# Optimization experiments

Hardware: AMD Instinct MI355X
Metric: run time of the kernel (lower is better)

Reference implementation:

```python
import jax, jax.numpy as jnp
import numpy as np

N_NODES = 100000
N_EDGES = 3200000
IN_DIM, HID, OUT = 512, 256, 64


def setup_inputs() -> dict:
    key = jax.random.key(0)
    k1, k2, k3, k4, k5, k6 = jax.random.split(key, 6)
    x = jax.random.normal(k1, (N_NODES, IN_DIM), dtype=jnp.float32)
    edge_src = jax.random.randint(k2, (N_EDGES,), 0, N_NODES, dtype=jnp.int32)
    edge_dst = jax.random.randint(k3, (N_EDGES,), 0, N_NODES, dtype=jnp.int32)
    edge_val = jax.random.uniform(k4, (N_EDGES,), dtype=jnp.float32)
    # glorot init as in the original `glorot([input_dim, output_dim])`
    w1 = jax.random.normal(k5, (IN_DIM, HID), dtype=jnp.float32) * np.sqrt(2.0 / (IN_DIM + HID))
    w2 = jax.random.normal(k6, (HID, OUT), dtype=jnp.float32) * np.sqrt(2.0 / (HID + OUT))
    return {"x": x, "edge_src": edge_src, "edge_dst": edge_dst,
            "edge_val": edge_val, "w1": w1, "w2": w2}


def _spmm(edge_src, edge_dst, edge_val, dense):
    # support @ dense : out[i] = sum_j A[i,j] * dense[j], A given as COO edges
    msgs = edge_val[:, None] * dense[edge_dst]            # [E, D] gather
    return jax.ops.segment_sum(msgs, edge_src, num_segments=N_NODES)  # scatter-add


def reference(x, edge_src, edge_dst, edge_val, w1, w2):
    # Layer 1: pre_sup = X @ W1 ; support = A @ pre_sup ; relu (no bias)
    h = jax.nn.relu(_spmm(edge_src, edge_dst, edge_val, x @ w1))  # [N, HID]
    # Layer 2: identity activation
    logits = _spmm(edge_src, edge_dst, edge_val, h @ w2)          # [N, OUT]
    return logits
```

## Files before the change

### kernel.cpp

```cpp
#include <hip/hip_runtime.h>

#define NN 100000
#define NE 3200000
#define IN_DIM 512
#define HID 256
#define OUTD 64
#define NB 196
#define CAP 20480
#define EPB 3125

typedef _Float16 f16x8 __attribute__((ext_vector_type(8)));
typedef float f32x4 __attribute__((ext_vector_type(4)));

__device__ __forceinline__ void async_copy16(void* lds, const void* g) {
    __builtin_amdgcn_global_load_lds(
        (const __attribute__((address_space(1))) void*)g,
        (__attribute__((address_space(3))) void*)lds, 16, 0, 0);
}

__device__ __forceinline__ void dq4(int w, float m, float* a) {
    int lo = (w & 0x00ff00ff) | 0x64006400;
    int hi = ((w >> 8) & 0x00ff00ff) | 0x64006400;
    asm("v_fma_mix_f32 %0, %1, %2, %0 op_sel:[0,0,0] op_sel_hi:[1,0,0]" : "+v"(a[0]) : "v"(lo), "v"(m));
    asm("v_fma_mix_f32 %0, %1, %2, %0 op_sel:[0,0,0] op_sel_hi:[1,0,0]" : "+v"(a[1]) : "v"(hi), "v"(m));
    asm("v_fma_mix_f32 %0, %1, %2, %0 op_sel:[1,0,0] op_sel_hi:[1,0,0]" : "+v"(a[2]) : "v"(lo), "v"(m));
    asm("v_fma_mix_f32 %0, %1, %2, %0 op_sel:[1,0,0] op_sel_hi:[1,0,0]" : "+v"(a[3]) : "v"(hi), "v"(m));
}


__global__ void prep_kernel(const float* __restrict__ w1, const float* __restrict__ w2,
                            _Float16* __restrict__ w1t, _Float16* __restrict__ w2t,
                            int* __restrict__ cursor) {
    int idx = blockIdx.x * blockDim.x + threadIdx.x;
    if (idx < NB) cursor[idx] = idx * CAP;
    if (idx < IN_DIM * HID) {
        int k = idx / HID, n = idx % HID;
        w1t[(size_t)n * IN_DIM + k] = (_Float16)w1[idx];
    } else if (idx < IN_DIM * HID + HID * OUTD) {
        int j = idx - IN_DIM * HID;
        int k = j / OUTD, n = j % OUTD;
        w2t[(size_t)n * HID + k] = (_Float16)w2[j];
    }
}


__global__ __launch_bounds__(256) void bin_kernel(const int* __restrict__ src,
                                                  const int* __restrict__ dst,
                                                  const float* __restrict__ val,
                                                  int* __restrict__ cursor,
                                                  int2* __restrict__ pairs_tmp,
                                                  int E) {
    __shared__ int s_src[EPB];
    __shared__ int s_dst[EPB];
    __shared__ int s_val[EPB];
    __shared__ int hist[NB];
    __shared__ int base[NB];
    const int t = threadIdx.x;
    const int lo = blockIdx.x * EPB;
    const int cnt = min(E - lo, EPB);
    for (int i = t; i < NB; i += 256) hist[i] = 0;
    for (int i = t; i < cnt; i += 256) {
        s_src[i] = src[lo + i];
        s_dst[i] = dst[lo + i];
        s_val[i] = __float_as_int(val[lo + i]);
    }
    __syncthreads();
    for (int i = t; i < cnt; i += 256) atomicAdd(&hist[s_src[i] >> 9], 1);
    __syncthreads();
    for (int i = t; i < NB; i += 256) {
        base[i] = atomicAdd(&cursor[i], hist[i]);
        hist[i] = 0;
    }
    __syncthreads();
    for (int i = t; i < cnt; i += 256) {
        int s = s_src[i];
        int b = s >> 9;
        int l = atomicAdd(&hist[b], 1);
        int pos = base[b] + l;
        pairs_tmp[pos] = make_int2(s_dst[i] | ((s & 511) << 20), s_val[i]);
    }
}


__global__ void bucket_scan_kernel(const int* __restrict__ cursor,
                                   int* __restrict__ bbase, int* __restrict__ offs) {
    __shared__ int sz[NB];
    int t = threadIdx.x;
    if (t < NB) sz[t] = cursor[t] - t * CAP;
    __syncthreads();
    if (t == 0) {
        int acc = 0;
        for (int i = 0; i < NB; ++i) { bbase[i] = acc; acc += sz[i]; }
        bbase[NB] = acc;
        offs[NN] = acc;
    }
}


#define CSR_LDS 18432
__global__ __launch_bounds__(1024) void csr_kernel(const int* __restrict__ cursor,
                                                   const int* __restrict__ bbase,
                                                   const int2* __restrict__ pairs_tmp,
                                                   const float* __restrict__ scales,
                                                   int* __restrict__ offs,
                                                   int2* __restrict__ pairs) {
    __shared__ int sx[CSR_LDS];
    __shared__ int sv[CSR_LDS];
    __shared__ int cnt[512];
    __shared__ int wsum[8];
    const int b = blockIdx.x;
    const int t = threadIdx.x;
    const int s0 = b << 9;
    const int base = bbase[b];
    const int n_b = cursor[b] - b * CAP;
    const int tlo = b * CAP;
    if (t < 512) cnt[t] = 0;
    __syncthreads();
    for (int i = t; i < n_b; i += 1024) {
        int2 pv = pairs_tmp[tlo + i];
        sx[i] = pv.x;
        sv[i] = pv.y;
        atomicAdd(&cnt[((unsigned)pv.x) >> 20], 1);
    }
    __syncthreads();
    int my = 0, incl = 0;
    if (t < 512) {
        my = cnt[t];
        incl = my;
        #pragma unroll
        for (int d = 1; d < 64; d <<= 1) {
            int y = __shfl_up(incl, d);
            if ((t & 63) >= d) incl += y;
        }
        if ((t & 63) == 63) wsum[t >> 6] = incl;
    }
    __syncthreads();
    if (t == 0) {
        int acc = 0;
        #pragma unroll
        for (int i = 0; i < 8; ++i) { int v = wsum[i]; wsum[i] = acc; acc += v; }
    }
    __syncthreads();
    if (t < 512) {
        int excl = base + incl - my + wsum[t >> 6];
        int s = s0 + t;
        if (s < NN) offs[s] = excl;
        cnt[t] = excl;
    }
    __syncthreads();
    for (int i = t; i < n_b; i += 1024) {
        int x = sx[i];
        int so = ((unsigned)x) >> 20;
        int p = atomicAdd(&cnt[so], 1);
        int dst = x & 0xFFFFF;
        float v = __int_as_float(sv[i]) * scales[dst];
        pairs[p] = make_int2(dst, __float_as_int(v));
    }
}


__global__ __launch_bounds__(256) void gemm1_f32a(const float* __restrict__ A,
                                                  const _Float16* __restrict__ Bt,
                                                  unsigned char* __restrict__ qC,
                                                  float* __restrict__ scales,
                                                  int M) {
    __shared__ float    As[128 * 32];
    __shared__ _Float16 Bs[256 * 32];
    __shared__ float    rmaxl[2][128];
    const int tid  = threadIdx.x;
    const int lane = tid & 63;
    const int wave = tid >> 6;
    const int wm = wave >> 1, wn = wave & 1;
    const int m0 = blockIdx.x * 128;

    f32x4 acc[4][8];
    #pragma unroll
    for (int i = 0; i < 4; ++i)
        #pragma unroll
        for (int j = 0; j < 8; ++j) acc[i][j] = (f32x4){0.f, 0.f, 0.f, 0.f};

    for (int k0 = 0; k0 < IN_DIM; k0 += 32) {
        #pragma unroll
        for (int it = 0; it < 4; ++it) {
            int i = it * 256 + tid;
            int r = i >> 3;
            int cp = i & 7;
            int cl = cp ^ (r & 7);
            int gr = m0 + r; if (gr >= M) gr = M - 1;
            async_copy16((char*)As + i * 16, A + (size_t)gr * IN_DIM + k0 + cl * 4);
        }
        #pragma unroll
        for (int it = 0; it < 4; ++it) {
            int i = it * 256 + tid;
            int r = i >> 2;
            int cp = i & 3;
            int cl = cp ^ (r & 3);
            async_copy16((char*)Bs + i * 16, Bt + (size_t)r * IN_DIM + k0 + cl * 8);
        }
        __syncthreads();

        const int kc = lane >> 4;
        f16x8 af[4];
        #pragma unroll
        for (int m = 0; m < 4; ++m) {
            int r = wm * 64 + m * 16 + (lane & 15);
            int p0 = (2 * kc) ^ (r & 7);
            int p1 = (2 * kc + 1) ^ (r & 7);
            f32x4 c0 = *(const f32x4*)((const char*)As + r * 128 + p0 * 16);
            f32x4 c1 = *(const f32x4*)((const char*)As + r * 128 + p1 * 16);
            f16x8 v = { (_Float16)c0[0], (_Float16)c0[1], (_Float16)c0[2], (_Float16)c0[3],
                        (_Float16)c1[0], (_Float16)c1[1], (_Float16)c1[2], (_Float16)c1[3] };
            af[m] = v;
        }
        f16x8 bf[8];
        #pragma unroll
        for (int n = 0; n < 8; ++n) {
            int r = wn * 128 + n * 16 + (lane & 15);
            bf[n] = *(const f16x8*)((const char*)Bs + r * 64 + ((kc ^ (r & 3)) * 16));
        }
        #pragma unroll
        for (int m = 0; m < 4; ++m)
            #pragma unroll
            for (int n = 0; n < 8; ++n)
                acc[m][n] = __builtin_amdgcn_mfma_f32_16x16x32_f16(af[m], bf[n], acc[m][n], 0, 0, 0);
        __syncthreads();
    }

    #pragma unroll
    for (int m = 0; m < 4; ++m)
        #pragma unroll
        for (int r = 0; r < 4; ++r) {
            float mm = 0.f;
            #pragma unroll
            for (int n = 0; n < 8; ++n) mm = fmaxf(mm, fabsf(acc[m][n][r]));
            #pragma unroll
            for (int d = 1; d < 16; d <<= 1) mm = fmaxf(mm, __shfl_xor(mm, d));
            if ((lane & 15) == 0)
                rmaxl[wn][wm * 64 + m * 16 + (lane >> 4) * 4 + r] = mm;
        }
    __syncthreads();
    #pragma unroll
    for (int m = 0; m < 4; ++m)
        #pragma unroll
        for (int r = 0; r < 4; ++r) {
            int lrow = wm * 64 + m * 16 + (lane >> 4) * 4 + r;
            int row = m0 + lrow;
            float full = fmaxf(fmaxf(rmaxl[0][lrow], rmaxl[1][lrow]), 1e-12f);
            float inv = 127.0f / full;
            if (row < M) {
                #pragma unroll
                for (int n = 0; n < 8; ++n) {
                    int col = wn * 128 + n * 16 + (lane & 15);
                    qC[(size_t)row * HID + col] =
                        (unsigned char)(__float2int_rn(acc[m][n][r] * inv) + 128);
                }
                if (wn == 0 && (lane & 15) == 0) scales[row] = full * (1.0f / 127.0f);
            }
        }
}


__global__ __launch_bounds__(256) void spmm_relu_mm2(const int* __restrict__ offs,
                                                     const int2* __restrict__ pairs,
                                                     const unsigned char* __restrict__ qpre,
                                                     const float* __restrict__ scales,
                                                     const _Float16* __restrict__ w2t,
                                                     unsigned char* __restrict__ qh2,
                                                     float* __restrict__ ratio2, int n) {
    __shared__ __align__(16) char hl_raw[16 * 528];
    __shared__ float rmax2[4][16];
    const int tid  = threadIdx.x;
    const int lane = tid & 63;
    const int wid  = tid >> 6;
    const int par  = lane >> 4;
    const int fl   = lane & 15;
    const int nbase = blockIdx.x * 16;
    const unsigned char* qbase = qpre + fl * 16;

    #pragma unroll 1
    for (int i = 0; i < 4; ++i) {
        const int node = nbase + wid * 4 + i;
        const int beg = offs[node], end = offs[node + 1];
        float a[16] = {};
        float msum = 0.f;
        int k = beg;
        for (; k + 16 <= end; k += 16) {
            int2 pr[4];
            #pragma unroll
            for (int j = 0; j < 4; ++j) pr[j] = pairs[k + 4 * j + par];
            int4 qv[4];
            #pragma unroll
            for (int j = 0; j < 4; ++j)
                qv[j] = *(const int4*)(qbase + (size_t)pr[j].x * HID);
            #pragma unroll
            for (int j = 0; j < 4; ++j) {
                float m = __int_as_float(pr[j].y);
                msum += m;
                dq4(qv[j].x, m, a + 0);
                dq4(qv[j].y, m, a + 4);
                dq4(qv[j].z, m, a + 8);
                dq4(qv[j].w, m, a + 12);
            }
        }
        if (k < end) {
            int2 pr[4];
            float m_[4];
            #pragma unroll
            for (int j = 0; j < 4; ++j) {
                int idx = k + 4 * j + par;
                int cidx = idx < end ? idx : end - 1;
                pr[j] = pairs[cidx];
                m_[j] = idx < end ? __int_as_float(pr[j].y) : 0.f;
            }
            int4 qv[4];
            #pragma unroll
            for (int j = 0; j < 4; ++j)
                qv[j] = *(const int4*)(qbase + (size_t)pr[j].x * HID);
            #pragma unroll
            for (int j = 0; j < 4; ++j) {
                float m = m_[j];
                msum += m;
                dq4(qv[j].x, m, a + 0);
                dq4(qv[j].y, m, a + 4);
                dq4(qv[j].z, m, a + 8);
                dq4(qv[j].w, m, a + 12);
            }
        }
        #pragma unroll
        for (int q = 0; q < 16; ++q) {
            a[q] += __shfl_xor(a[q], 16);
            a[q] += __shfl_xor(a[q], 32);
        }
        msum += __shfl_xor(msum, 16);
        msum += __shfl_xor(msum, 32);
        if (par == 0) {
            float bias = 1152.f * msum;
            f16x8 o0, o1;
            #pragma unroll
            for (int q = 0; q < 8; ++q) {
                o0[q] = (_Float16)fmaxf(a[q] - bias, 0.f);
                o1[q] = (_Float16)fmaxf(a[8 + q] - bias, 0.f);
            }
            char* bp = hl_raw + (wid * 4 + i) * 528 + fl * 16;
            *(f16x8*)bp         = o0;
            *(f16x8*)(bp + 256) = o1;
        }
    }
    __syncthreads();

    const int r  = lane & 15;
    const int kc = lane >> 4;
    f32x4 acc = (f32x4){0.f, 0.f, 0.f, 0.f};
    #pragma unroll
    for (int kk = 0; kk < 8; ++kk) {
        int c = kk * 4 + kc;
        f16x8 af = *(const f16x8*)(hl_raw + r * 528 + ((c & 1) << 8) + ((c >> 1) << 4));
        f16x8 bf = *(const f16x8*)(w2t + (size_t)(wid * 16 + r) * HID + kk * 32 + kc * 8);
        acc = __builtin_amdgcn_mfma_f32_16x16x32_f16(af, bf, acc, 0, 0, 0);
    }
    float mxv[4];
    #pragma unroll
    for (int j = 0; j < 4; ++j) {
        float mm = fabsf(acc[j]);
        #pragma unroll
        for (int d = 1; d < 16; d <<= 1) mm = fmaxf(mm, __shfl_xor(mm, d));
        mxv[j] = mm;
    }
    if (r == 0) {
        #pragma unroll
        for (int j = 0; j < 4; ++j) rmax2[wid][kc * 4 + j] = mxv[j];
    }
    __syncthreads();
    #pragma unroll
    for (int j = 0; j < 4; ++j) {
        int ln = kc * 4 + j;
        int node = nbase + ln;
        float full = fmaxf(fmaxf(fmaxf(rmax2[0][ln], rmax2[1][ln]),
                                 fmaxf(rmax2[2][ln], rmax2[3][ln])), 1e-12f);
        qh2[(size_t)node * OUTD + wid * 16 + r] =
            (unsigned char)(__float2int_rn(acc[j] * (127.0f / full)) + 128);
        if (wid == 0 && r == 0)
            ratio2[node] = full * (1.0f / 127.0f) / scales[node];
    }
}


__global__ __launch_bounds__(256) void spmm64_q(const int* __restrict__ offs,
                                                const int2* __restrict__ pairs,
                                                const unsigned char* __restrict__ qh2,
                                                const float* __restrict__ ratio2,
                                                float* __restrict__ out, int n) {
    int node = blockIdx.x * 4 + (threadIdx.x >> 6);
    if (node >= n) return;
    int lane = threadIdx.x & 63;
    int par = lane >> 2;
    int fl  = lane & 3;
    int beg = offs[node], end = offs[node + 1];
    const unsigned char* qbase = qh2 + fl * 16;
    float a[16] = {};
    float msum = 0.f;
    int k = beg;
    for (; k + 32 <= end; k += 32) {
        int2 pr[2];
        #pragma unroll
        for (int j = 0; j < 2; ++j) pr[j] = pairs[k + 16 * j + par];
        float rt[2];
        #pragma unroll
        for (int j = 0; j < 2; ++j) rt[j] = ratio2[pr[j].x];
        int4 qv[2];
        #pragma unroll
        for (int j = 0; j < 2; ++j)
            qv[j] = *(const int4*)(qbase + (size_t)pr[j].x * OUTD);
        #pragma unroll
        for (int j = 0; j < 2; ++j) {
            float m = __int_as_float(pr[j].y) * rt[j];
            msum += m;
            dq4(qv[j].x, m, a + 0);
            dq4(qv[j].y, m, a + 4);
            dq4(qv[j].z, m, a + 8);
            dq4(qv[j].w, m, a + 12);
        }
    }
    if (k < end) {
        int2 pr[2];
        float m_[2];
        #pragma unroll
        for (int j = 0; j < 2; ++j) {
            int idx = k + 16 * j + par;
            int cidx = idx < end ? idx : end - 1;
            pr[j] = pairs[cidx];
            m_[j] = idx < end ? __int_as_float(pr[j].y) * ratio2[pr[j].x] : 0.f;
        }
        int4 qv[2];
        #pragma unroll
        for (int j = 0; j < 2; ++j)
            qv[j] = *(const int4*)(qbase + (size_t)pr[j].x * OUTD);
        #pragma unroll
        for (int j = 0; j < 2; ++j) {
            float m = m_[j];
            msum += m;
            dq4(qv[j].x, m, a + 0);
            dq4(qv[j].y, m, a + 4);
            dq4(qv[j].z, m, a + 8);
            dq4(qv[j].w, m, a + 12);
        }
    }
    #pragma unroll
    for (int q = 0; q < 16; ++q) {
        a[q] += __shfl_xor(a[q], 4);
        a[q] += __shfl_xor(a[q], 8);
        a[q] += __shfl_xor(a[q], 16);
        a[q] += __shfl_xor(a[q], 32);
    }
    msum += __shfl_xor(msum, 4);
    msum += __shfl_xor(msum, 8);
    msum += __shfl_xor(msum, 16);
    msum += __shfl_xor(msum, 32);
    if (par == 0) {
        float bias = 1152.f * msum;
        float* ob = out + (size_t)node * OUTD + fl * 16;
        #pragma unroll
        for (int c = 0; c < 4; ++c) {
            float4 o = make_float4(a[4 * c] - bias, a[4 * c + 1] - bias,
                                   a[4 * c + 2] - bias, a[4 * c + 3] - bias);
            *(float4*)(ob + 4 * c) = o;
        }
    }
}


extern "C" void kernel_launch(void* const* d_in, const int* in_sizes, int n_in,
                              void* d_out, int out_size, void* d_ws, size_t ws_size,
                              hipStream_t stream) {
    const float* x    = (const float*)d_in[0];
    const int*   esrc = (const int*)d_in[1];
    const int*   edst = (const int*)d_in[2];
    const float* eval = (const float*)d_in[3];
    const float* w1   = (const float*)d_in[4];
    const float* w2   = (const float*)d_in[5];
    float* out = (float*)d_out;

    char* ws = (char*)d_ws;
    unsigned char* qpre   = (unsigned char*)(ws + 0);
    unsigned char* qh2    = (unsigned char*)(ws + 25600000);
    float*        scales  = (float*)(ws + 32000000);
    float*        ratio2  = (float*)(ws + 32400000);
    int2*         pairs   = (int2*)(ws + 32800000);
    int2*         pairs_t = (int2*)(ws + 58400000);
    int*          cursor  = (int*)(ws + 90512640);
    int*          bbase   = (int*)(ws + 90513664);
    int*          offs    = (int*)(ws + 90514688);
    _Float16*     w1t     = (_Float16*)(ws + 90914816);
    _Float16*     w2t     = (_Float16*)(ws + 91176960);

    prep_kernel<<<(IN_DIM * HID + HID * OUTD + 255) / 256, 256, 0, stream>>>(w1, w2, w1t, w2t, cursor);

    bin_kernel<<<1024, 256, 0, stream>>>(esrc, edst, eval, cursor, pairs_t, NE);

    bucket_scan_kernel<<<1, 256, 0, stream>>>(cursor, bbase, offs);

    gemm1_f32a<<<(NN + 127) / 128, 256, 0, stream>>>(x, w1t, qpre, scales, NN);

    csr_kernel<<<NB, 1024, 0, stream>>>(cursor, bbase, pairs_t, scales, offs, pairs);

    spmm_relu_mm2<<<NN / 16, 256, 0, stream>>>(offs, pairs, qpre, scales, w2t, qh2, ratio2, NN);

    spmm64_q<<<(NN + 3) / 4, 256, 0, stream>>>(offs, pairs, qh2, ratio2, out, NN);
}
```

Baseline: 405.8 us.

## Double-buffer gemm1 LDS tiles and halve the row tile to 64

The first GEMM kernel now double-buffers its A and B tiles in shared memory, issuing the async global-to-LDS copies for the next K slice before computing on the current one. This hides load latency behind the MFMA work. The M tile also shrinks from 128 to 64 rows, so the grid doubles, each block uses fewer accumulator registers and occupancy can rise. In exchange, W1 tiles are reloaded twice as often per row of output. There is still only one barrier per iteration, so correct overlap depends on how async LDS writes are tracked against that barrier.

```diff
diff --git a/kernel.cpp b/kernel.cpp
--- a/kernel.cpp
+++ b/kernel.cpp
@@ -164,50 +164,55 @@
                                                   unsigned char* __restrict__ qC,
                                                   float* __restrict__ scales,
                                                   int M) {
-    __shared__ float    As[128 * 32];
-    __shared__ _Float16 Bs[256 * 32];
-    __shared__ float    rmaxl[2][128];
+    __shared__ float    As[2][64 * 32];
+    __shared__ _Float16 Bs[2][256 * 32];
+    __shared__ float    rmaxl[2][64];
     const int tid  = threadIdx.x;
     const int lane = tid & 63;
     const int wave = tid >> 6;
     const int wm = wave >> 1, wn = wave & 1;
-    const int m0 = blockIdx.x * 128;
-
-    f32x4 acc[4][8];
-    #pragma unroll
-    for (int i = 0; i < 4; ++i)
+    const int m0 = blockIdx.x * 64;
+
+    f32x4 acc[2][8];
+    #pragma unroll
+    for (int i = 0; i < 2; ++i)
         #pragma unroll
         for (int j = 0; j < 8; ++j) acc[i][j] = (f32x4){0.f, 0.f, 0.f, 0.f};
 
-    for (int k0 = 0; k0 < IN_DIM; k0 += 32) {
-        #pragma unroll
-        for (int it = 0; it < 4; ++it) {
+    auto stage = [&](int b, int k0) {
+        #pragma unroll
+        for (int it = 0; it < 2; ++it) {
             int i = it * 256 + tid;
             int r = i >> 3;
-            int cp = i & 7;
-            int cl = cp ^ (r & 7);
+            int cl = (i & 7) ^ (r & 7);
             int gr = m0 + r; if (gr >= M) gr = M - 1;
-            async_copy16((char*)As + i * 16, A + (size_t)gr * IN_DIM + k0 + cl * 4);
+            async_copy16((char*)As[b] + i * 16, A + (size_t)gr * IN_DIM + k0 + cl * 4);
         }
         #pragma unroll
         for (int it = 0; it < 4; ++it) {
             int i = it * 256 + tid;
             int r = i >> 2;
-            int cp = i & 3;
-            int cl = cp ^ (r & 3);
-            async_copy16((char*)Bs + i * 16, Bt + (size_t)r * IN_DIM + k0 + cl * 8);
-        }
-        __syncthreads();
-
-        const int kc = lane >> 4;
-        f16x8 af[4];
-        #pragma unroll
-        for (int m = 0; m < 4; ++m) {
-            int r = wm * 64 + m * 16 + (lane & 15);
+            int cl = (i & 3) ^ (r & 3);
+            async_copy16((char*)Bs[b] + i * 16, Bt + (size_t)r * IN_DIM + k0 + cl * 8);
+        }
+    };
+
+    stage(0, 0);
+    __syncthreads();
+
+    int cur = 0;
+    const int kc = lane >> 4;
+    for (int t = 0; t < IN_DIM / 32; ++t) {
+        if (t + 1 < IN_DIM / 32) stage(cur ^ 1, (t + 1) * 32);
+
+        f16x8 af[2];
+        #pragma unroll
+        for (int m = 0; m < 2; ++m) {
+            int r = wm * 32 + m * 16 + (lane & 15);
             int p0 = (2 * kc) ^ (r & 7);
             int p1 = (2 * kc + 1) ^ (r & 7);
-            f32x4 c0 = *(const f32x4*)((const char*)As + r * 128 + p0 * 16);
-            f32x4 c1 = *(const f32x4*)((const char*)As + r * 128 + p1 * 16);
+            f32x4 c0 = *(const f32x4*)((const char*)As[cur] + r * 128 + p0 * 16);
+            f32x4 c1 = *(const f32x4*)((const char*)As[cur] + r * 128 + p1 * 16);
             f16x8 v = { (_Float16)c0[0], (_Float16)c0[1], (_Float16)c0[2], (_Float16)c0[3],
                         (_Float16)c1[0], (_Float16)c1[1], (_Float16)c1[2], (_Float16)c1[3] };
             af[m] = v;
@@ -216,18 +221,20 @@
         #pragma unroll
         for (int n = 0; n < 8; ++n) {
             int r = wn * 128 + n * 16 + (lane & 15);
-            bf[n] = *(const f16x8*)((const char*)Bs + r * 64 + ((kc ^ (r & 3)) * 16));
-        }
-        #pragma unroll
-        for (int m = 0; m < 4; ++m)
+            bf[n] = *(const f16x8*)((const char*)Bs[cur] + r * 64 + ((kc ^ (r & 3)) * 16));
+        }
+        #pragma unroll
+        for (int m = 0; m < 2; ++m)
             #pragma unroll
             for (int n = 0; n < 8; ++n)
                 acc[m][n] = __builtin_amdgcn_mfma_f32_16x16x32_f16(af[m], bf[n], acc[m][n], 0, 0, 0);
+
         __syncthreads();
-    }
-
-    #pragma unroll
-    for (int m = 0; m < 4; ++m)
+        cur ^= 1;
+    }
+
+    #pragma unroll
+    for (int m = 0; m < 2; ++m)
         #pragma unroll
         for (int r = 0; r < 4; ++r) {
             float mm = 0.f;
@@ -236,14 +243,14 @@
             #pragma unroll
             for (int d = 1; d < 16; d <<= 1) mm = fmaxf(mm, __shfl_xor(mm, d));
             if ((lane & 15) == 0)
-                rmaxl[wn][wm * 64 + m * 16 + (lane >> 4) * 4 + r] = mm;
-        }
-    __syncthreads();
-    #pragma unroll
-    for (int m = 0; m < 4; ++m)
+                rmaxl[wn][wm * 32 + m * 16 + kc * 4 + r] = mm;
+        }
+    __syncthreads();
+    #pragma unroll
+    for (int m = 0; m < 2; ++m)
         #pragma unroll
         for (int r = 0; r < 4; ++r) {
-            int lrow = wm * 64 + m * 16 + (lane >> 4) * 4 + r;
+            int lrow = wm * 32 + m * 16 + kc * 4 + r;
             int row = m0 + lrow;
             float full = fmaxf(fmaxf(rmaxl[0][lrow], rmaxl[1][lrow]), 1e-12f);
             float inv = 127.0f / full;
@@ -499,7 +506,7 @@
 
     bucket_scan_kernel<<<1, 256, 0, stream>>>(cursor, bbase, offs);
 
-    gemm1_f32a<<<(NN + 127) / 128, 256, 0, stream>>>(x, w1t, qpre, scales, NN);
+    gemm1_f32a<<<(NN + 63) / 64, 256, 0, stream>>>(x, w1t, qpre, scales, NN);
 
     csr_kernel<<<NB, 1024, 0, stream>>>(cursor, bbase, pairs_t, scales, offs, pairs);
 
```

Measured after the change: 385.3 us. -5.1%, faster.
